# Kernel tuning notes

Hardware: AMD Instinct MI355X
Metric: run time of the kernel (lower is better)

The kernel has to match this reference:

```python
import jax, jax.numpy as jnp
import numpy as np
import math

B, T, C = 4, 2048, 768
N_HEAD = 12
HEAD_DIM = C // N_HEAD


def setup_inputs() -> dict:
    key = jax.random.key(0)
    k1, k2, k3, k4, k5 = jax.random.split(key, 5)
    std = 0.02
    x = jax.random.normal(k1, (B, T, C), dtype=jnp.float32)
    W_attn = jax.random.normal(k2, (C, 3 * C), dtype=jnp.float32) * std
    b_attn = jnp.zeros((3 * C,), dtype=jnp.float32)
    W_proj = jax.random.normal(k3, (C, C), dtype=jnp.float32) * std
    b_proj = jnp.zeros((C,), dtype=jnp.float32)
    return {"x": x, "W_attn": W_attn, "b_attn": b_attn,
            "W_proj": W_proj, "b_proj": b_proj}


def reference(x, W_attn, b_attn, W_proj, b_proj):
    b, t, c = x.shape
    h, hd = N_HEAD, c // N_HEAD
    # qkv projection: [B,T,3C] -> q,k,v each [B,H,T,hd]
    qkv = x @ W_attn + b_attn
    qkv = qkv.reshape(b, t, 3, h, hd).transpose(2, 0, 3, 1, 4)  # [3,B,H,T,hd]
    q, k, v = qkv[0], qkv[1], qkv[2]
    scale = 1.0 / math.sqrt(hd)
    # full T x T attention scores (non-flash, as in original)
    attn = jnp.einsum('bhqd,bhkd->bhqk', q, k) * scale  # [B,H,T,T]
    causal = jnp.tril(jnp.ones((t, t), dtype=bool))
    attn = jnp.where(causal[None, None, :, :], attn, -jnp.inf)
    attn = jax.nn.softmax(attn, axis=-1)
    y = jnp.einsum('bhqk,bhkd->bhqd', attn, v)  # [B,H,T,hd]
    y = y.transpose(0, 2, 1, 3).reshape(b, t, c)  # merge heads
    return y @ W_proj + b_proj
```

## Files before the change

### kernel.cpp

```cpp
#include <hip/hip_runtime.h>
#include <hip/hip_bf16.h>
#include <cstdint>

#define B_  4
#define T_  2048
#define C_  768
#define H_  12
#define HD_ 64

#define AS1 __attribute__((address_space(1)))
#define AS3 __attribute__((address_space(3)))

typedef float    f32x4  __attribute__((ext_vector_type(4)));
typedef __bf16   bf16x8 __attribute__((ext_vector_type(8)));
typedef uint32_t u32x4  __attribute__((ext_vector_type(4)));

#define QSCL 0.18033688011112042f
#define MFIX 8.0f

__device__ __forceinline__ uint16_t f2b(float f) {
  __bf16 h = (__bf16)f;
  return __builtin_bit_cast(uint16_t, h);
}
__device__ __forceinline__ uint32_t pk2(float a, float b) {
  return (uint32_t)f2b(a) | ((uint32_t)f2b(b) << 16);
}

__global__ void k_cvt(const float* __restrict__ in, uint16_t* __restrict__ out, int n4) {
  int i = blockIdx.x * blockDim.x + threadIdx.x;
  if (i >= n4) return;
  float4 v = ((const float4*)in)[i];
  uint2 o;
  o.x = pk2(v.x, v.y);
  o.y = pk2(v.z, v.w);
  ((uint2*)out)[i] = o;
}

__global__ void k_tr(const float* __restrict__ in, uint16_t* __restrict__ out, int R, int Cc) {
  __shared__ float tile[32][33];
  int n0 = blockIdx.x * 32, k0 = blockIdx.y * 32;
  int tx = threadIdx.x, ty = threadIdx.y;
#pragma unroll
  for (int i = 0; i < 32; i += 8)
    tile[ty + i][tx] = in[(size_t)(k0 + ty + i) * Cc + n0 + tx];
  __syncthreads();
#pragma unroll
  for (int i = 0; i < 32; i += 8)
    out[(size_t)(n0 + ty + i) * R + k0 + tx] = f2b(tile[tx][ty + i]);
}

template <int EPI>
__global__ __launch_bounds__(256, 3) void k_gemm(
    const uint16_t* __restrict__ A, const uint16_t* __restrict__ Bt,
    const float* __restrict__ bias, float* __restrict__ outF,
    uint16_t* __restrict__ outQKV, int M, int N, int K) {
  __shared__ __align__(16) uint16_t As[2][128 * 32];
  __shared__ __align__(16) uint16_t Bs[2][128 * 32];
  const int tid  = threadIdx.x;
  const int lane = tid & 63;
  const int wave = tid >> 6;
  const int wrow = (wave >> 1) * 64, wcol = (wave & 1) * 64;
  const int rowBase = blockIdx.x * 128, colBase = blockIdx.y * 128;
  const int l16 = lane & 15, kg = lane >> 4;

  f32x4 acc[4][4];
#pragma unroll
  for (int i = 0; i < 4; ++i)
#pragma unroll
    for (int j = 0; j < 4; ++j) acc[i][j] = (f32x4){0.f, 0.f, 0.f, 0.f};

  const int srow  = lane >> 2;
  const int sslot = lane & 3;
  const int ssw   = (sslot ^ (srow & 3)) << 3;

  auto STAGE = [&](int buf, int k0) {
#pragma unroll
    for (int i = 0; i < 2; ++i) {
      const int r = i * 64 + wave * 16 + srow;
      const uint16_t* srcA = A  + (size_t)(rowBase + r) * K + k0 + ssw;
      const uint16_t* srcB = Bt + (size_t)(colBase + r) * K + k0 + ssw;
      uint16_t* dstA = &As[buf][(i * 64 + wave * 16) * 32];
      uint16_t* dstB = &Bs[buf][(i * 64 + wave * 16) * 32];
      __builtin_amdgcn_global_load_lds((const AS1 uint32_t*)srcA, (AS3 uint32_t*)dstA, 16, 0, 0);
      __builtin_amdgcn_global_load_lds((const AS1 uint32_t*)srcB, (AS3 uint32_t*)dstB, 16, 0, 0);
    }
  };

  const int sA = (kg ^ (l16 & 3)) << 3;

  STAGE(0, 0);
  int cur = 0;
  for (int k0 = 0; k0 < K; k0 += 32) {
    __syncthreads();
    if (k0 + 32 < K) STAGE(cur ^ 1, k0 + 32);
    bf16x8 af[4], bfv[4];
#pragma unroll
    for (int mi = 0; mi < 4; ++mi)
      af[mi] = *(const bf16x8*)&As[cur][(wrow + mi * 16 + l16) * 32 + sA];
#pragma unroll
    for (int nj = 0; nj < 4; ++nj)
      bfv[nj] = *(const bf16x8*)&Bs[cur][(wcol + nj * 16 + l16) * 32 + sA];
#pragma unroll
    for (int mi = 0; mi < 4; ++mi)
#pragma unroll
      for (int nj = 0; nj < 4; ++nj)
        acc[mi][nj] = __builtin_amdgcn_mfma_f32_16x16x32_bf16(af[mi], bfv[nj], acc[mi][nj], 0, 0, 0);
    cur ^= 1;
  }

  const int rg = lane >> 4;
#pragma unroll
  for (int mi = 0; mi < 4; ++mi)
#pragma unroll
    for (int nj = 0; nj < 4; ++nj) {
      int c = colBase + wcol + nj * 16 + l16;
      float bv = bias[c];
#pragma unroll
      for (int jj = 0; jj < 4; ++jj) {
        int r = rowBase + wrow + mi * 16 + rg * 4 + jj;
        float v = acc[mi][nj][jj] + bv;
        if (EPI == 0) {
          outF[(size_t)r * N + c] = v;
        } else {
          int sel = c / 768;
          int rem = c - sel * 768;
          int head = rem >> 6, d = rem & 63;
          int bb = r >> 11, tt = r & 2047;
          size_t off;
          if (sel == 2)
            off = (((size_t)2 * (B_ * H_) + bb * H_ + head) * HD_ + d) * T_ + tt;
          else
            off = (((size_t)sel * (B_ * H_) + bb * H_ + head) * T_ + tt) * HD_ + d;
          if (sel == 0) v *= QSCL;
          outQKV[off] = f2b(v);
        }
      }
    }
}

__global__ __launch_bounds__(256, 4) void k_attn2(
    const uint16_t* __restrict__ Qb, const uint16_t* __restrict__ Kb,
    const uint16_t* __restrict__ Vb, uint16_t* __restrict__ Y) {
  __shared__ __align__(16) uint16_t Ks[2][64 * 64];
  __shared__ __align__(16) uint16_t Vs[2][64 * 64];
  __shared__ __align__(16) uint16_t Ps[4][16 * 64];
  const int tid  = threadIdx.x;
  const int lane = tid & 63;
  const int wq   = tid >> 6;
  const int l16  = lane & 15, kg = lane >> 4;
  const int px = blockIdx.x, h = blockIdx.y, b = blockIdx.z;
  const size_t headBase = ((size_t)(b * H_ + h)) * (size_t)(T_ * HD_);

  const int srow0 = wq * 16 + (lane >> 3);
  const int sslot = lane & 7;
  const int swz = (l16 & 7) << 2;

  uint32_t* pwords = (uint32_t*)&Ps[wq][0];

  auto STAGE = [&](int buf, int t) {
    const int kvoff = t * 64;
#pragma unroll
    for (int j = 0; j < 2; ++j) {
      const int r  = srow0 + j * 8;
      const int sw = ((sslot ^ (r & 7)) << 3);
      const uint16_t* srcK = Kb + headBase + (size_t)(kvoff + r) * HD_ + sw;
      const uint16_t* srcV = Vb + headBase + (size_t)r * T_ + kvoff + sw;
      uint16_t* dstK = &Ks[buf][(wq * 16 + j * 8) * 64];
      uint16_t* dstV = &Vs[buf][(wq * 16 + j * 8) * 64];
      __builtin_amdgcn_global_load_lds((const AS1 uint32_t*)srcK, (AS3 uint32_t*)dstK, 16, 0, 0);
      __builtin_amdgcn_global_load_lds((const AS1 uint32_t*)srcV, (AS3 uint32_t*)dstV, 16, 0, 0);
    }
  };

  int cur = 0;
  for (int part = 0; part < 2; ++part) {
    const int qb = part ? (31 - px) : px;
    const int qrow0 = qb * 64 + wq * 16;

    bf16x8 qf[2];
    {
      const uint16_t* qp = Qb + headBase + (size_t)(qrow0 + l16) * HD_;
      qf[0] = *(const bf16x8*)(qp + kg * 8);
      qf[1] = *(const bf16x8*)(qp + 32 + kg * 8);
    }

    f32x4 o[4];
#pragma unroll
    for (int i = 0; i < 4; ++i) o[i] = (f32x4){0.f, 0.f, 0.f, 0.f};
    float l_ = 0.f;

    const int nt = qb + 1;
    __syncthreads();
    STAGE(cur, 0);

    for (int t = 0; t < nt; ++t) {
      __syncthreads();
      if (t + 1 < nt) STAGE(cur ^ 1, t + 1);

      const uint16_t* KT = &Ks[cur][0];
      const uint16_t* VT = &Vs[cur][0];

      f32x4 sm[4];
      __builtin_amdgcn_s_setprio(1);
#pragma unroll
      for (int nj = 0; nj < 4; ++nj) {
        f32x4 acc = (f32x4){0.f, 0.f, 0.f, 0.f};
#pragma unroll
        for (int kc = 0; kc < 2; ++kc) {
          const int row = nj * 16 + l16;
          const int s = (((kc * 4 + kg) ^ (row & 7)) << 3);
          bf16x8 kf = *(const bf16x8*)&KT[row * 64 + s];
          acc = __builtin_amdgcn_mfma_f32_16x16x32_bf16(kf, qf[kc], acc, 0, 0, 0);
        }
        sm[nj] = acc;
      }
      __builtin_amdgcn_s_setprio(0);

      if (t == qb) {
        const int kvb = t * 64 + kg * 4;
        const int qg  = qrow0 + l16;
#pragma unroll
        for (int nj = 0; nj < 4; ++nj)
#pragma unroll
          for (int jj = 0; jj < 4; ++jj)
            if (kvb + nj * 16 + jj > qg) sm[nj][jj] = -__builtin_inff();
      }

#pragma unroll
      for (int nj = 0; nj < 4; ++nj) {
#pragma unroll
        for (int jj = 0; jj < 4; ++jj) {
          float p = __builtin_exp2f(sm[nj][jj] - MFIX);
          sm[nj][jj] = p;
          l_ += p;
        }
      }

#pragma unroll
      for (int nj = 0; nj < 4; ++nj) {
        uint2 w;
        w.x = pk2(sm[nj][0], sm[nj][1]);
        w.y = pk2(sm[nj][2], sm[nj][3]);
        const int cs = (nj * 8 + kg * 2) ^ swz;
        *(uint2*)&pwords[l16 * 32 + cs] = w;
      }

      __builtin_amdgcn_s_setprio(1);
#pragma unroll
      for (int kc = 0; kc < 2; ++kc) {
        const int cr = (kc * 16 + kg * 4) ^ swz;
        bf16x8 pa = *(const bf16x8*)&pwords[l16 * 32 + cr];
#pragma unroll
        for (int njd = 0; njd < 4; ++njd) {
          const int row = njd * 16 + l16;
          const int s = (((kc * 4 + kg) ^ (row & 7)) << 3);
          bf16x8 vf = *(const bf16x8*)&VT[row * 64 + s];
          o[njd] = __builtin_amdgcn_mfma_f32_16x16x32_bf16(vf, pa, o[njd], 0, 0, 0);
        }
      }
      __builtin_amdgcn_s_setprio(0);

      cur ^= 1;
    }

    l_ += __shfl_xor(l_, 16);
    l_ += __shfl_xor(l_, 32);
    float inv = __builtin_amdgcn_rcpf(l_);
    const int q = qrow0 + l16;
    uint16_t* yp = Y + ((size_t)(b * T_ + q)) * C_ + h * HD_ + kg * 4;
#pragma unroll
    for (int njd = 0; njd < 4; ++njd) {
      uint2 w;
      w.x = pk2(o[njd][0] * inv, o[njd][1] * inv);
      w.y = pk2(o[njd][2] * inv, o[njd][3] * inv);
      *(uint2*)(yp + njd * 16) = w;
    }
  }
}

extern "C" void kernel_launch(void* const* d_in, const int* in_sizes, int n_in,
                              void* d_out, int out_size, void* d_ws, size_t ws_size,
                              hipStream_t stream) {
  const float* x      = (const float*)d_in[0];
  const float* W_attn = (const float*)d_in[1];
  const float* b_attn = (const float*)d_in[2];
  const float* W_proj = (const float*)d_in[3];
  const float* b_proj = (const float*)d_in[4];
  float* out = (float*)d_out;

  char* ws = (char*)d_ws;
  uint16_t* xb  = (uint16_t*)(ws);
  uint16_t* WtA = (uint16_t*)(ws + 12582912);
  uint16_t* WtP = (uint16_t*)(ws + 16121856);
  uint16_t* QKV = (uint16_t*)(ws + 17301504);
  uint16_t* Yb  = (uint16_t*)(ws + 55050240);

  uint16_t* Qp = QKV;
  uint16_t* Kp = QKV + 6291456;
  uint16_t* Vp = QKV + 12582912;

  k_cvt<<<6144, 256, 0, stream>>>(x, xb, 1572864);
  k_tr<<<dim3(72, 24), dim3(32, 8), 0, stream>>>(W_attn, WtA, 768, 2304);
  k_tr<<<dim3(24, 24), dim3(32, 8), 0, stream>>>(W_proj, WtP, 768, 768);
  k_gemm<1><<<dim3(64, 18), 256, 0, stream>>>(xb, WtA, b_attn, nullptr, QKV, 8192, 2304, 768);
  k_attn2<<<dim3(16, 12, 4), 256, 0, stream>>>(Qp, Kp, Vp, Yb);
  k_gemm<0><<<dim3(64, 6), 256, 0, stream>>>(Yb, WtP, b_proj, out, nullptr, 8192, 768, 768);
}
```

Before: 160.6 us.

## Remap workgroup IDs for XCD-aware L2 locality and merge weight transposes

Launches the GEMMs and attention on 1D grids and remaps block IDs so that consecutive blocks sent to the same XCD (bid & 7) share row/column tiles or attention heads. The goal is better L2 reuse across the chiplets. The two weight-transpose kernels are fused into one launch to cut launch overhead. The softmax row-sum becomes a vector accumulator reduced once at the end, which shortens the serial add chain. The remap assumes grid sizes divisible by 8.

Result: no change. 158.2 us (-1.5%).

```diff
diff --git a/kernel.cpp b/kernel.cpp
--- a/kernel.cpp
+++ b/kernel.cpp
@@ -36,31 +36,43 @@
   ((uint2*)out)[i] = o;
 }
 
-__global__ void k_tr(const float* __restrict__ in, uint16_t* __restrict__ out, int R, int Cc) {
+__global__ void k_tr2(const float* __restrict__ Wa, uint16_t* __restrict__ WtA,
+                      const float* __restrict__ Wp, uint16_t* __restrict__ WtP) {
   __shared__ float tile[32][33];
-  int n0 = blockIdx.x * 32, k0 = blockIdx.y * 32;
-  int tx = threadIdx.x, ty = threadIdx.y;
+  const int bx = blockIdx.x;
+  const float* in;
+  uint16_t* out;
+  int Cc, n0;
+  if (bx < 72) { in = Wa; out = WtA; Cc = 2304; n0 = bx * 32; }
+  else         { in = Wp; out = WtP; Cc = 768;  n0 = (bx - 72) * 32; }
+  const int k0 = blockIdx.y * 32;
+  const int tx = threadIdx.x, ty = threadIdx.y;
 #pragma unroll
   for (int i = 0; i < 32; i += 8)
     tile[ty + i][tx] = in[(size_t)(k0 + ty + i) * Cc + n0 + tx];
   __syncthreads();
 #pragma unroll
   for (int i = 0; i < 32; i += 8)
-    out[(size_t)(n0 + ty + i) * R + k0 + tx] = f2b(tile[tx][ty + i]);
+    out[(size_t)(n0 + ty + i) * 768 + k0 + tx] = f2b(tile[tx][ty + i]);
 }
 
 template <int EPI>
 __global__ __launch_bounds__(256, 3) void k_gemm(
     const uint16_t* __restrict__ A, const uint16_t* __restrict__ Bt,
     const float* __restrict__ bias, float* __restrict__ outF,
-    uint16_t* __restrict__ outQKV, int M, int N, int K) {
+    uint16_t* __restrict__ outQKV, int M, int N, int K, int nY) {
   __shared__ __align__(16) uint16_t As[2][128 * 32];
   __shared__ __align__(16) uint16_t Bs[2][128 * 32];
+  const int nwg = gridDim.x;
+  const int bid = blockIdx.x;
+  const int wgid = (bid & 7) * (nwg >> 3) + (bid >> 3);
+  const int wy = wgid % nY, wx = wgid / nY;
+
   const int tid  = threadIdx.x;
   const int lane = tid & 63;
   const int wave = tid >> 6;
   const int wrow = (wave >> 1) * 64, wcol = (wave & 1) * 64;
-  const int rowBase = blockIdx.x * 128, colBase = blockIdx.y * 128;
+  const int rowBase = wx * 128, colBase = wy * 128;
   const int l16 = lane & 15, kg = lane >> 4;
 
   f32x4 acc[4][4];
@@ -148,7 +160,12 @@
   const int lane = tid & 63;
   const int wq   = tid >> 6;
   const int l16  = lane & 15, kg = lane >> 4;
-  const int px = blockIdx.x, h = blockIdx.y, b = blockIdx.z;
+
+  const int idx = blockIdx.x;
+  const int tq  = idx >> 3;
+  const int px  = tq & 15;
+  const int g   = (idx & 7) + 8 * (tq >> 4);
+  const int h = g % H_, b = g / H_;
   const size_t headBase = ((size_t)(b * H_ + h)) * (size_t)(T_ * HD_);
 
   const int srow0 = wq * 16 + (lane >> 3);
@@ -187,7 +204,7 @@
     f32x4 o[4];
 #pragma unroll
     for (int i = 0; i < 4; ++i) o[i] = (f32x4){0.f, 0.f, 0.f, 0.f};
-    float l_ = 0.f;
+    f32x4 lacc = (f32x4){0.f, 0.f, 0.f, 0.f};
 
     const int nt = qb + 1;
     __syncthreads();
@@ -229,11 +246,9 @@
 #pragma unroll
       for (int nj = 0; nj < 4; ++nj) {
 #pragma unroll
-        for (int jj = 0; jj < 4; ++jj) {
-          float p = __builtin_exp2f(sm[nj][jj] - MFIX);
-          sm[nj][jj] = p;
-          l_ += p;
-        }
+        for (int jj = 0; jj < 4; ++jj)
+          sm[nj][jj] = __builtin_exp2f(sm[nj][jj] - MFIX);
+        lacc += sm[nj];
       }
 
 #pragma unroll
@@ -263,6 +278,7 @@
       cur ^= 1;
     }
 
+    float l_ = (lacc[0] + lacc[1]) + (lacc[2] + lacc[3]);
     l_ += __shfl_xor(l_, 16);
     l_ += __shfl_xor(l_, 32);
     float inv = __builtin_amdgcn_rcpf(l_);
@@ -300,9 +316,8 @@
   uint16_t* Vp = QKV + 12582912;
 
   k_cvt<<<6144, 256, 0, stream>>>(x, xb, 1572864);
-  k_tr<<<dim3(72, 24), dim3(32, 8), 0, stream>>>(W_attn, WtA, 768, 2304);
-  k_tr<<<dim3(24, 24), dim3(32, 8), 0, stream>>>(W_proj, WtP, 768, 768);
-  k_gemm<1><<<dim3(64, 18), 256, 0, stream>>>(xb, WtA, b_attn, nullptr, QKV, 8192, 2304, 768);
-  k_attn2<<<dim3(16, 12, 4), 256, 0, stream>>>(Qp, Kp, Vp, Yb);
-  k_gemm<0><<<dim3(64, 6), 256, 0, stream>>>(Yb, WtP, b_proj, out, nullptr, 8192, 768, 768);
-}
+  k_tr2<<<dim3(96, 24), dim3(32, 8), 0, stream>>>(W_attn, WtA, W_proj, WtP);
+  k_gemm<1><<<1152, 256, 0, stream>>>(xb, WtA, b_attn, nullptr, QKV, 8192, 2304, 768, 18);
+  k_attn2<<<768, 256, 0, stream>>>(Qp, Kp, Vp, Yb);
+  k_gemm<0><<<384, 256, 0, stream>>>(Yb, WtP, b_proj, out, nullptr, 8192, 768, 768, 6);
+}
```
